# Performance work log

Hardware: AMD Instinct MI355X
Metric: run time of the kernel (lower is better)

The kernel has to match this reference:

```python
import jax, jax.numpy as jnp
import numpy as np

L, B, T, D, H = 8, 4, 1024, 1024, 16
DH = D // H
TPB, NB = 16, 64  # tokens_per_block, max_blocks; T == TPB*NB
EPS = 1e-5


def _block_causal_mask():
    idx = jnp.arange(T)
    causal = idx[:, None] >= idx[None, :]
    blk = idx // TPB
    block_diag = blk[:, None] == blk[None, :]
    return causal | block_diag  # [T, T] bool


def _ln(x, g, b):
    mu = jnp.mean(x, axis=-1, keepdims=True)
    var = jnp.mean(jnp.square(x - mu), axis=-1, keepdims=True)
    return (x - mu) * jax.lax.rsqrt(var + EPS) * g + b


def setup_inputs() -> dict:
    key = jax.random.key(0)
    ks = jax.random.split(key, 8)
    s = 0.02
    inp = {
        'sequences': jax.random.normal(ks[0], (B, T, D), jnp.float32),
        'Wq': jax.random.normal(ks[1], (L, D, D), jnp.float32) * s,
        'bq': jnp.zeros((L, D), jnp.float32),
        'Wk': jax.random.normal(ks[2], (L, D, D), jnp.float32) * s,
        'bk': jnp.zeros((L, D), jnp.float32),
        'Wv': jax.random.normal(ks[3], (L, D, D), jnp.float32) * s,
        'bv': jnp.zeros((L, D), jnp.float32),
        'Wp': jax.random.normal(ks[4], (L, D, D), jnp.float32) * s,
        'bp': jnp.zeros((L, D), jnp.float32),
        'ln1_g': jnp.ones((L, D), jnp.float32),
        'ln1_b': jnp.zeros((L, D), jnp.float32),
        'ln2_g': jnp.ones((L, D), jnp.float32),
        'ln2_b': jnp.zeros((L, D), jnp.float32),
        'W1': jax.random.normal(ks[5], (L, D, 4 * D), jnp.float32) * s,
        'b1': jnp.zeros((L, 4 * D), jnp.float32),
        'W2': jax.random.normal(ks[6], (L, 4 * D, D), jnp.float32) * s,
        'b2': jnp.zeros((L, D), jnp.float32),
        'lnf_g': jnp.ones((D,), jnp.float32),
        'lnf_b': jnp.zeros((D,), jnp.float32),
    }
    return inp


def reference(sequences, Wq, bq, Wk, bk, Wv, bv, Wp, bp,
              ln1_g, ln1_b, ln2_g, ln2_b, W1, b1, W2, b2, lnf_g, lnf_b):
    mask = _block_causal_mask()
    scale = 1.0 / np.sqrt(DH)
    x = sequences
    for i in range(L):
        h = _ln(x, ln1_g[i], ln1_b[i])
        q = (h @ Wq[i] + bq[i]).reshape(B, T, H, DH)
        k = (h @ Wk[i] + bk[i]).reshape(B, T, H, DH)
        v = (h @ Wv[i] + bv[i]).reshape(B, T, H, DH)
        att = jnp.einsum('bthd,bshd->bhts', q, k) * scale  # [B,H,T,T]
        att = jnp.where(mask, att, -jnp.inf)
        att = jax.nn.softmax(att, axis=-1)
        y = jnp.einsum('bhts,bshd->bthd', att, v).reshape(B, T, D)
        x = x + (y @ Wp[i] + bp[i])
        h2 = _ln(x, ln2_g[i], ln2_b[i])
        ff = jax.nn.gelu(h2 @ W1[i] + b1[i], approximate=False) @ W2[i] + b2[i]
        x = x + ff
    return _ln(x, lnf_g, lnf_b)
```

## Files before the change

kernel.cpp:

```cpp
#include <hip/hip_runtime.h>
#include <hip/hip_bf16.h>
#include <math.h>

#define B_ 4
#define T_ 1024
#define D_ 1024
#define H_ 16
#define DH_ 64
#define M_ 4096
#define QSTR_ 3072
#define EPS_ 1e-5f

typedef __attribute__((ext_vector_type(4))) float f32x4;
typedef __attribute__((ext_vector_type(8))) short s16x8;

#if __has_builtin(__builtin_amdgcn_exp2f)
#define EXP2F __builtin_amdgcn_exp2f
#else
#define EXP2F exp2f
#endif

__device__ __forceinline__ float gelu_f(float x) {
  return 0.5f * x * (1.0f + erff(x * 0.70710678118654752f));
}
__device__ __forceinline__ float b2f(unsigned short u) {
  union { unsigned int i; float f; } c; c.i = ((unsigned int)u) << 16; return c.f;
}
__device__ __forceinline__ unsigned short f2b(float f) {
  __hip_bfloat16 h = __float2bfloat16(f);
  return *reinterpret_cast<unsigned short*>(&h);
}
__device__ __forceinline__ void g2l16(void* l, const void* g) {
  __builtin_amdgcn_global_load_lds(
      (const __attribute__((address_space(1))) void*)g,
      (__attribute__((address_space(3))) void*)l, 16, 0, 0);
}

template<bool BF16OUT>
__global__ __launch_bounds__(256) void ln_kernel(
    const float* __restrict__ in, void* __restrict__ out,
    const float* __restrict__ g, const float* __restrict__ b) {
  const int row = blockIdx.x;
  const int tid = threadIdx.x;
  const float* rp = in + (size_t)row * D_;
  float4 v = *reinterpret_cast<const float4*>(rp + tid * 4);
  float s = v.x + v.y + v.z + v.w;
  float s2 = v.x * v.x + v.y * v.y + v.z * v.z + v.w * v.w;
#pragma unroll
  for (int off = 1; off < 64; off <<= 1) {
    s += __shfl_xor(s, off);
    s2 += __shfl_xor(s2, off);
  }
  __shared__ float red[2][4];
  const int wid = tid >> 6;
  if ((tid & 63) == 0) { red[0][wid] = s; red[1][wid] = s2; }
  __syncthreads();
  s = red[0][0] + red[0][1] + red[0][2] + red[0][3];
  s2 = red[1][0] + red[1][1] + red[1][2] + red[1][3];
  const float mu = s * (1.0f / D_);
  const float var = s2 * (1.0f / D_) - mu * mu;
  const float rs = rsqrtf(var + EPS_);
  float4 gv = *reinterpret_cast<const float4*>(g + tid * 4);
  float4 bv = *reinterpret_cast<const float4*>(b + tid * 4);
  float o0 = (v.x - mu) * rs * gv.x + bv.x;
  float o1 = (v.y - mu) * rs * gv.y + bv.y;
  float o2 = (v.z - mu) * rs * gv.z + bv.z;
  float o3 = (v.w - mu) * rs * gv.w + bv.w;
  if (BF16OUT) {
    ushort4 pk;
    pk.x = f2b(o0); pk.y = f2b(o1); pk.z = f2b(o2); pk.w = f2b(o3);
    *reinterpret_cast<ushort4*>((unsigned short*)out + (size_t)row * D_ + tid * 4) = pk;
  } else {
    *reinterpret_cast<float4*>((float*)out + (size_t)row * D_ + tid * 4) =
        make_float4(o0, o1, o2, o3);
  }
}

__global__ __launch_bounds__(256) void concat_bias(
    const float* __restrict__ bq, const float* __restrict__ bk,
    const float* __restrict__ bv, float* __restrict__ out) {
  const int i = blockIdx.x * 256 + threadIdx.x;
  const int l = i / QSTR_, c = i % QSTR_;
  const float* src = (c < 1024) ? bq : ((c < 2048) ? bk : bv);
  out[i] = src[l * 1024 + (c & 1023)];
}

__device__ __forceinline__ void transpose_tile(
    const float* __restrict__ src, int sld,
    __hip_bfloat16* __restrict__ dst, int dld, int k0, int n0) {
  __shared__ float tile[32][33];
  const int t = threadIdx.x;
  const int r = t >> 3;
  const int cq = (t & 7) * 4;
  float4 vv = *reinterpret_cast<const float4*>(src + (size_t)(k0 + r) * sld + n0 + cq);
  tile[r][cq + 0] = vv.x; tile[r][cq + 1] = vv.y;
  tile[r][cq + 2] = vv.z; tile[r][cq + 3] = vv.w;
  __syncthreads();
  ushort4 o;
  o.x = f2b(tile[cq + 0][r]); o.y = f2b(tile[cq + 1][r]);
  o.z = f2b(tile[cq + 2][r]); o.w = f2b(tile[cq + 3][r]);
  *reinterpret_cast<ushort4*>((unsigned short*)dst + (size_t)(n0 + r) * dld + k0 + cq) = o;
}

struct TrAll {
  const float *wq, *wk, *wv, *wp, *w1, *w2;
  __hip_bfloat16 *dqkv, *dp, *d1, *d2;
};

__global__ __launch_bounds__(256) void transpose_all(TrAll a) {
  const int t = blockIdx.x;
  const float* src;
  __hip_bfloat16* dst;
  int sld, dld, k0, n0;
  if (t < 4096) {
    const int m = t >> 10, tile = t & 1023;
    k0 = (tile >> 5) * 32; n0 = (tile & 31) * 32;
    src = (m == 0) ? a.wq : (m == 1) ? a.wk : (m == 2) ? a.wv : a.wp;
    sld = 1024; dld = 1024;
    dst = (m < 3) ? (a.dqkv + (size_t)m * 1024 * 1024) : a.dp;
  } else if (t < 8192) {
    const int tile = t - 4096;
    k0 = (tile & 31) * 32; n0 = (tile >> 5) * 32;
    src = a.w1; sld = 4096; dst = a.d1; dld = 1024;
  } else {
    const int tile = t - 8192;
    k0 = (tile >> 5) * 32; n0 = (tile & 31) * 32;
    src = a.w2; sld = 1024; dst = a.d2; dld = 4096;
  }
  transpose_tile(src, sld, dst, dld, k0, n0);
}

template<int MODE, int BN>
__global__ __launch_bounds__(256) void gemm_mfma(
    const __hip_bfloat16* __restrict__ A,
    const __hip_bfloat16* __restrict__ Bt,
    const float* __restrict__ bias,
    void* __restrict__ Cout, int N, int K) {
  __shared__ short As[3][128 * 32];
  __shared__ short Bs[3][BN * 32];
  int bid = blockIdx.y * gridDim.x + blockIdx.x;
  const int nwg = gridDim.x * gridDim.y;
  bid = (bid & 7) * (nwg >> 3) + (bid >> 3);
  const int gn = (bid % gridDim.x) * BN;
  const int gm = (bid / gridDim.x) * 128;

  const int tid = threadIdx.x;
  const int wid = tid >> 6, lane = tid & 63;
  constexpr int MR = (BN == 128) ? 4 : 2;
  const int wm = (BN == 128) ? (wid >> 1) : wid;
  const int wn = (BN == 128) ? (wid & 1) : 0;
  const int fr = lane & 15, kg = lane >> 4;

  const int ldr = lane >> 2;
  const int ldk = (((lane & 3) ^ ((lane >> 3) & 3)) * 8);
  const unsigned short* ap =
      (const unsigned short*)A + (size_t)(gm + wid * 32 + ldr) * K + ldk;
  const unsigned short* bp =
      (const unsigned short*)Bt +
      (size_t)(gn + ((BN == 128) ? wid * 32 : wid * 16) + ldr) * K + ldk;

  const int nkt = K >> 5;

#define STAGE_T(t, buf)                                                    \
  {                                                                        \
    const unsigned short* a_ = ap + (size_t)(t) * 32;                      \
    g2l16((char*)As[buf] + (wid * 2) * 1024, a_);                          \
    g2l16((char*)As[buf] + (wid * 2 + 1) * 1024, a_ + (size_t)16 * K);     \
    const unsigned short* b_ = bp + (size_t)(t) * 32;                      \
    if (BN == 128) {                                                       \
      g2l16((char*)Bs[buf] + (wid * 2) * 1024, b_);                        \
      g2l16((char*)Bs[buf] + (wid * 2 + 1) * 1024, b_ + (size_t)16 * K);   \
    } else {                                                               \
      g2l16((char*)Bs[buf] + wid * 1024, b_);                              \
    }                                                                      \
  }

  STAGE_T(0, 0);
  STAGE_T(1, 1);

  const int cxa = (kg ^ ((fr >> 1) & 3)) * 8;
  f32x4 acc[MR][4] = {};
  for (int t = 0; t < nkt; ++t) {
    const int buf = t % 3;
    if (t + 2 < nkt) STAGE_T(t + 2, (t + 2) % 3);
    const int rem = nkt - 1 - t;
    if (rem >= 2) {
      if (BN == 128) asm volatile("s_waitcnt vmcnt(8)" ::: "memory");
      else           asm volatile("s_waitcnt vmcnt(6)" ::: "memory");
    } else if (rem == 1) {
      if (BN == 128) asm volatile("s_waitcnt vmcnt(4)" ::: "memory");
      else           asm volatile("s_waitcnt vmcnt(3)" ::: "memory");
    } else {
      asm volatile("s_waitcnt vmcnt(0)" ::: "memory");
    }
    __builtin_amdgcn_s_barrier();
    __builtin_amdgcn_sched_barrier(0);
    s16x8 af[MR], bfr[4];
#pragma unroll
    for (int m = 0; m < MR; ++m)
      af[m] = *reinterpret_cast<const s16x8*>(
          &As[buf][(wm * (16 * MR) + m * 16 + fr) * 32 + cxa]);
#pragma unroll
    for (int n = 0; n < 4; ++n)
      bfr[n] = *reinterpret_cast<const s16x8*>(
          &Bs[buf][(wn * 64 + n * 16 + fr) * 32 + cxa]);
#pragma unroll
    for (int m = 0; m < MR; ++m)
#pragma unroll
      for (int n = 0; n < 4; ++n)
        acc[m][n] = __builtin_amdgcn_mfma_f32_16x16x32_bf16(af[m], bfr[n], acc[m][n], 0, 0, 0);
    __builtin_amdgcn_sched_barrier(0);
    __builtin_amdgcn_s_barrier();
  }
#undef STAGE_T

  const int r0 = gm + wm * (16 * MR);
  const int c0 = gn + wn * 64;
  float bb[4];
#pragma unroll
  for (int n = 0; n < 4; ++n)
    bb[n] = bias ? bias[c0 + n * 16 + fr] : 0.0f;
#pragma unroll
  for (int m = 0; m < MR; ++m) {
#pragma unroll
    for (int j = 0; j < 4; ++j) {
      const int row = r0 + m * 16 + kg * 4 + j;
#pragma unroll
      for (int n = 0; n < 4; ++n) {
        float val = acc[m][n][j] + bb[n];
        const size_t idx = (size_t)row * N + c0 + n * 16 + fr;
        if (MODE == 0) {
          ((unsigned short*)Cout)[idx] = f2b(val);
        } else if (MODE == 1) {
          float* cp = (float*)Cout + idx;
          *cp = *cp + val;
        } else {
          ((unsigned short*)Cout)[idx] = f2b(gelu_f(val));
        }
      }
    }
  }
}

__global__ __launch_bounds__(256) void attn_mfma(
    const __hip_bfloat16* __restrict__ qkv, __hip_bfloat16* __restrict__ yg) {
  const int qb = 7 - blockIdx.x;
  const int hh = blockIdx.y;
  const int bb = blockIdx.z;
  __shared__ short Qs[128 * 64];
  __shared__ short Ks[64 * 64];
  __shared__ short Vt[64 * 64];
  const int tid = threadIdx.x;
  const int wid = tid >> 6, lane = tid & 63;
  const int fr = lane & 15, kg = lane >> 4;
  const size_t qb_base = (size_t)bb * T_ * QSTR_ + (size_t)hh * DH_;
  const unsigned short* qgp = (const unsigned short*)qkv + qb_base;
  const unsigned short* kgp = qgp + 1024;
  const unsigned short* vgp = qgp + 2048;
  const float C = 0.125f * 1.4426950408889634f;

  {
    const int r8 = lane >> 3, cp = lane & 7;
#pragma unroll
    for (int u = 0; u < 4; ++u) {
      const int row = wid * 32 + u * 8 + r8;
      const int c16 = cp ^ (row & 7);
      g2l16((char*)Qs + (wid * 32 + u * 8) * 128,
            qgp + (size_t)(qb * 128 + row) * QSTR_ + c16 * 8);
    }
  }
  asm volatile("s_waitcnt vmcnt(0)" ::: "memory");
  __syncthreads();
  s16x8 qf[2][2];
#pragma unroll
  for (int rg = 0; rg < 2; ++rg) {
    const int row = wid * 32 + rg * 16 + fr;
    const char* rp = (const char*)Qs + row * 128;
    qf[rg][0] = *reinterpret_cast<const s16x8*>(rp + (((0 + kg) ^ (row & 7)) << 4));
    qf[rg][1] = *reinterpret_cast<const s16x8*>(rp + (((4 + kg) ^ (row & 7)) << 4));
  }

  f32x4 acco[2][4] = {};
  float m_run[2][4], l_run[2][4];
#pragma unroll
  for (int rg = 0; rg < 2; ++rg)
#pragma unroll
    for (int j = 0; j < 4; ++j) { m_run[rg][j] = -INFINITY; l_run[rg][j] = 0.f; }

  const int q16hi = qb * 8 + wid * 2 + 1;
  const int ntile = 2 * qb + 2;
  for (int kt = 0; kt < ntile; ++kt) {
    __syncthreads();
    {
      const int r8 = lane >> 3, cp = lane & 7;
#pragma unroll
      for (int u = 0; u < 2; ++u) {
        const int row = wid * 16 + u * 8 + r8;
        const int c16 = cp ^ (row & 7);
        g2l16((char*)Ks + (wid * 16 + u * 8) * 128,
              kgp + (size_t)(kt * 64 + row) * QSTR_ + c16 * 8);
      }
    }
    {
      const int kv0 = tid >> 3;
      const int d0 = (tid & 7) * 8;
      const int rot = tid & 7;
#pragma unroll
      for (int u = 0; u < 2; ++u) {
        const int kv = u * 32 + kv0;
        s16x8 sv = *reinterpret_cast<const s16x8*>(
            vgp + (size_t)(kt * 64 + kv) * QSTR_ + d0);
#pragma unroll
        for (int j = 0; j < 8; ++j) {
          const int jj = (j + rot) & 7;
          const int d = d0 + jj;
          *(short*)((char*)Vt + d * 128 + ((((kv >> 3) ^ jj) & 7) << 4) + (kv & 7) * 2) = sv[jj];
        }
      }
    }
    asm volatile("s_waitcnt vmcnt(0)" ::: "memory");
    __syncthreads();

    if (kt * 4 <= q16hi) {
      f32x4 accs[2][4] = {};
#pragma unroll
      for (int n = 0; n < 4; ++n) {
        const int row = n * 16 + fr;
        const char* rp = (const char*)Ks + row * 128;
        s16x8 kf0 = *reinterpret_cast<const s16x8*>(rp + (((0 + kg) ^ (row & 7)) << 4));
        s16x8 kf1 = *reinterpret_cast<const s16x8*>(rp + (((4 + kg) ^ (row & 7)) << 4));
#pragma unroll
        for (int rg = 0; rg < 2; ++rg) {
          accs[rg][n] = __builtin_amdgcn_mfma_f32_16x16x32_bf16(qf[rg][0], kf0, accs[rg][n], 0, 0, 0);
          accs[rg][n] = __builtin_amdgcn_mfma_f32_16x16x32_bf16(qf[rg][1], kf1, accs[rg][n], 0, 0, 0);
        }
      }
#pragma unroll
      for (int rg = 0; rg < 2; ++rg) {
        const int q16 = qb * 8 + wid * 2 + rg;
        float mloc[4] = {-3.0e38f, -3.0e38f, -3.0e38f, -3.0e38f};
#pragma unroll
        for (int n = 0; n < 4; ++n)
          if (kt * 4 + n <= q16)
#pragma unroll
            for (int j = 0; j < 4; ++j) mloc[j] = fmaxf(mloc[j], accs[rg][n][j]);
#pragma unroll
        for (int off = 1; off < 16; off <<= 1)
#pragma unroll
          for (int j = 0; j < 4; ++j) mloc[j] = fmaxf(mloc[j], __shfl_xor(mloc[j], off));
        float a_[4];
#pragma unroll
        for (int j = 0; j < 4; ++j) {
          const float mn = fmaxf(m_run[rg][j], mloc[j]);
          a_[j] = EXP2F((m_run[rg][j] - mn) * C);
          m_run[rg][j] = mn;
        }
        float psum[4] = {};
#pragma unroll
        for (int n = 0; n < 4; ++n) {
          const bool dead = (kt * 4 + n > q16);
          const int c16b = n * 2 + (fr >> 3);
#pragma unroll
          for (int j = 0; j < 4; ++j) {
            float p = dead ? 0.0f : EXP2F((accs[rg][n][j] - m_run[rg][j]) * C);
            psum[j] += p;
            const int row = wid * 32 + rg * 16 + kg * 4 + j;
            *(short*)((char*)Qs + row * 128 + (((c16b ^ (row & 7)) & 7) << 4) + (fr & 7) * 2) =
                (short)f2b(p);
          }
        }
#pragma unroll
        for (int j = 0; j < 4; ++j) l_run[rg][j] = l_run[rg][j] * a_[j] + psum[j];
#pragma unroll
        for (int dt = 0; dt < 4; ++dt)
#pragma unroll
          for (int j = 0; j < 4; ++j) acco[rg][dt][j] *= a_[j];
      }
#pragma unroll
      for (int rg = 0; rg < 2; ++rg) {
        const int prow = wid * 32 + rg * 16 + fr;
        const char* pp = (const char*)Qs + prow * 128;
#pragma unroll
        for (int kk = 0; kk < 2; ++kk) {
          const s16x8 pf = *reinterpret_cast<const s16x8*>(
              pp + ((((kk * 4 + kg) ^ (prow & 7)) & 7) << 4));
#pragma unroll
          for (int dt = 0; dt < 4; ++dt) {
            const int vrow = dt * 16 + fr;
            const s16x8 vf = *reinterpret_cast<const s16x8*>(
                (const char*)Vt + vrow * 128 + ((((kk * 4 + kg) ^ (vrow & 7)) & 7) << 4));
            acco[rg][dt] = __builtin_amdgcn_mfma_f32_16x16x32_bf16(pf, vf, acco[rg][dt], 0, 0, 0);
          }
        }
      }
    }
  }

#pragma unroll
  for (int off = 1; off < 16; off <<= 1)
#pragma unroll
    for (int rg = 0; rg < 2; ++rg)
#pragma unroll
      for (int j = 0; j < 4; ++j) l_run[rg][j] += __shfl_xor(l_run[rg][j], off);
  unsigned short* yp = (unsigned short*)yg + (size_t)bb * T_ * D_ + (size_t)hh * DH_;
#pragma unroll
  for (int rg = 0; rg < 2; ++rg) {
    float inv[4];
#pragma unroll
    for (int j = 0; j < 4; ++j) inv[j] = 1.0f / l_run[rg][j];
#pragma unroll
    for (int dt = 0; dt < 4; ++dt)
#pragma unroll
      for (int j = 0; j < 4; ++j) {
        const int row = qb * 128 + wid * 32 + rg * 16 + kg * 4 + j;
        yp[(size_t)row * D_ + dt * 16 + fr] = f2b(acco[rg][dt][j] * inv[j]);
      }
  }
}

extern "C" void kernel_launch(void* const* d_in, const int* in_sizes, int n_in,
                              void* d_out, int out_size, void* d_ws, size_t ws_size,
                              hipStream_t stream) {
  (void)in_sizes; (void)n_in; (void)out_size; (void)ws_size;
  const float* seq  = (const float*)d_in[0];
  const float* Wq   = (const float*)d_in[1];
  const float* bq   = (const float*)d_in[2];
  const float* Wk   = (const float*)d_in[3];
  const float* bk   = (const float*)d_in[4];
  const float* Wv   = (const float*)d_in[5];
  const float* bv   = (const float*)d_in[6];
  const float* Wp   = (const float*)d_in[7];
  const float* bp   = (const float*)d_in[8];
  const float* ln1g = (const float*)d_in[9];
  const float* ln1b = (const float*)d_in[10];
  const float* ln2g = (const float*)d_in[11];
  const float* ln2b = (const float*)d_in[12];
  const float* W1   = (const float*)d_in[13];
  const float* b1   = (const float*)d_in[14];
  const float* W2   = (const float*)d_in[15];
  const float* b2   = (const float*)d_in[16];
  const float* lnfg = (const float*)d_in[17];
  const float* lnfb = (const float*)d_in[18];

  float* x = (float*)d_out;
  char* ws = (char*)d_ws;
  const size_t MB = 1024ull * 1024ull;
  typedef __hip_bfloat16 bf16;
  bf16*  wtqkv = (bf16*)(ws + 0 * MB);
  bf16*  wtp   = (bf16*)(ws + 6 * MB);
  bf16*  wtF1  = (bf16*)(ws + 8 * MB);
  bf16*  wtF2  = (bf16*)(ws + 16 * MB);
  bf16*  hb    = (bf16*)(ws + 24 * MB);
  bf16*  qkv   = (bf16*)(ws + 32 * MB);
  bf16*  mid   = (bf16*)(ws + 56 * MB);
  float* bqkv  = (float*)(ws + 88 * MB);

  hipMemcpyAsync(x, seq, (size_t)M_ * D_ * sizeof(float), hipMemcpyDeviceToDevice, stream);

  const dim3 blk(256);
  concat_bias<<<96, blk, 0, stream>>>(bq, bk, bv, bqkv);

  for (int i = 0; i < 8; ++i) {
    const size_t wo  = (size_t)i * D_ * D_;
    const size_t vo  = (size_t)i * D_;
    const size_t w1o = (size_t)i * D_ * 4 * D_;

    ln_kernel<true><<<M_, blk, 0, stream>>>(x, hb, ln1g + vo, ln1b + vo);
    TrAll ta;
    ta.wq = Wq + wo; ta.wk = Wk + wo; ta.wv = Wv + wo; ta.wp = Wp + wo;
    ta.w1 = W1 + w1o; ta.w2 = W2 + w1o;
    ta.dqkv = wtqkv; ta.dp = wtp; ta.d1 = wtF1; ta.d2 = wtF2;
    transpose_all<<<12288, blk, 0, stream>>>(ta);
    gemm_mfma<0, 128><<<dim3(24, 32), blk, 0, stream>>>(
        hb, wtqkv, bqkv + (size_t)i * QSTR_, qkv, QSTR_, 1024);
    attn_mfma<<<dim3(8, 16, 4), blk, 0, stream>>>(qkv, hb);
    gemm_mfma<1, 64><<<dim3(16, 32), blk, 0, stream>>>(hb, wtp, bp + vo, x, 1024, 1024);
    ln_kernel<true><<<M_, blk, 0, stream>>>(x, hb, ln2g + vo, ln2b + vo);
    gemm_mfma<2, 128><<<dim3(32, 32), blk, 0, stream>>>(
        hb, wtF1, b1 + (size_t)i * 4096, mid, 4096, 1024);
    gemm_mfma<1, 64><<<dim3(16, 32), blk, 0, stream>>>(
        mid, wtF2, b2 + vo, x, 1024, 4096);
  }
  ln_kernel<false><<<M_, blk, 0, stream>>>(x, x, lnfg, lnfb);
}
```

Measured before the change: 2.292 ms.

## Split-K the FFN down-projection GEMM into two halves plus a reduction kernel

Replaces the FFN second GEMM (K=4096, 512 workgroups) with a split-K kernel that launches 1024 workgroups, each covering half of K. The first split adds its result and the bias into x, the second writes partials to a scratch buffer that reuses the qkv workspace, and a separate kernel then adds those partials into x. The aim is more parallelism and shorter per-block K loops, at the cost of an extra 16MB write, an extra read-modify-write pass over x, and one more launch per layer.

```diff
diff --git a/kernel.cpp b/kernel.cpp
--- a/kernel.cpp
+++ b/kernel.cpp
@@ -85,6 +85,15 @@
   out[i] = src[l * 1024 + (c & 1023)];
 }
 
+__global__ __launch_bounds__(256) void reduce_add(
+    float* __restrict__ x, const float* __restrict__ p) {
+  const int i = blockIdx.x * 256 + threadIdx.x;
+  float4 a = reinterpret_cast<float4*>(x)[i];
+  float4 b = reinterpret_cast<const float4*>(p)[i];
+  a.x += b.x; a.y += b.y; a.z += b.z; a.w += b.w;
+  reinterpret_cast<float4*>(x)[i] = a;
+}
+
 __device__ __forceinline__ void transpose_tile(
     const float* __restrict__ src, int sld,
     __hip_bfloat16* __restrict__ dst, int dld, int k0, int n0) {
@@ -239,6 +248,108 @@
         }
       }
     }
+  }
+}
+
+__global__ __launch_bounds__(256) void gemm_sk2(
+    const __hip_bfloat16* __restrict__ A,
+    const __hip_bfloat16* __restrict__ Bt,
+    const float* __restrict__ bias,
+    float* __restrict__ X, float* __restrict__ P,
+    int N, int K , int KS ) {
+  __shared__ short As[3][128 * 32];
+  __shared__ short Bs[3][64 * 32];
+  int bid = blockIdx.y * gridDim.x + blockIdx.x;
+  const int nwg = gridDim.x * gridDim.y;
+  bid = (bid & 7) * (nwg >> 3) + (bid >> 3);
+  const int gn = (bid % gridDim.x) * 64;
+  const int gm = (bid / gridDim.x) * 128;
+  const int koff = blockIdx.z * KS;
+
+  const int tid = threadIdx.x;
+  const int wid = tid >> 6, lane = tid & 63;
+  const int wm = wid, wn = 0;
+  const int fr = lane & 15, kg = lane >> 4;
+
+  const int ldr = lane >> 2;
+  const int ldk = (((lane & 3) ^ ((lane >> 3) & 3)) * 8);
+  const unsigned short* ap =
+      (const unsigned short*)A + (size_t)(gm + wid * 32 + ldr) * K + koff + ldk;
+  const unsigned short* bp =
+      (const unsigned short*)Bt + (size_t)(gn + wid * 16 + ldr) * K + koff + ldk;
+
+  const int nkt = KS >> 5;
+
+#define STAGE_S(t, buf)                                                    \
+  {                                                                        \
+    const unsigned short* a_ = ap + (size_t)(t) * 32;                      \
+    g2l16((char*)As[buf] + (wid * 2) * 1024, a_);                          \
+    g2l16((char*)As[buf] + (wid * 2 + 1) * 1024, a_ + (size_t)16 * K);     \
+    g2l16((char*)Bs[buf] + wid * 1024, bp + (size_t)(t) * 32);             \
+  }
+
+  STAGE_S(0, 0);
+  STAGE_S(1, 1);
+
+  const int cxa = (kg ^ ((fr >> 1) & 3)) * 8;
+  f32x4 acc[2][4] = {};
+  for (int t = 0; t < nkt; ++t) {
+    const int buf = t % 3;
+    if (t + 2 < nkt) STAGE_S(t + 2, (t + 2) % 3);
+    const int rem = nkt - 1 - t;
+    if (rem >= 2)      asm volatile("s_waitcnt vmcnt(6)" ::: "memory");
+    else if (rem == 1) asm volatile("s_waitcnt vmcnt(3)" ::: "memory");
+    else               asm volatile("s_waitcnt vmcnt(0)" ::: "memory");
+    __builtin_amdgcn_s_barrier();
+    __builtin_amdgcn_sched_barrier(0);
+    s16x8 af[2], bfr[4];
+#pragma unroll
+    for (int m = 0; m < 2; ++m)
+      af[m] = *reinterpret_cast<const s16x8*>(
+          &As[buf][(wm * 32 + m * 16 + fr) * 32 + cxa]);
+#pragma unroll
+    for (int n = 0; n < 4; ++n)
+      bfr[n] = *reinterpret_cast<const s16x8*>(
+          &Bs[buf][(wn * 64 + n * 16 + fr) * 32 + cxa]);
+#pragma unroll
+    for (int m = 0; m < 2; ++m)
+#pragma unroll
+      for (int n = 0; n < 4; ++n)
+        acc[m][n] = __builtin_amdgcn_mfma_f32_16x16x32_bf16(af[m], bfr[n], acc[m][n], 0, 0, 0);
+    __builtin_amdgcn_sched_barrier(0);
+    __builtin_amdgcn_s_barrier();
+  }
+#undef STAGE_S
+
+  const int r0 = gm + wm * 32;
+  const int c0 = gn;
+  if (blockIdx.z == 0) {
+    float bb[4];
+#pragma unroll
+    for (int n = 0; n < 4; ++n) bb[n] = bias[c0 + n * 16 + fr];
+#pragma unroll
+    for (int m = 0; m < 2; ++m)
+#pragma unroll
+      for (int j = 0; j < 4; ++j) {
+        const int row = r0 + m * 16 + kg * 4 + j;
+#pragma unroll
+        for (int n = 0; n < 4; ++n) {
+          const size_t idx = (size_t)row * N + c0 + n * 16 + fr;
+          X[idx] = X[idx] + acc[m][n][j] + bb[n];
+        }
+      }
+  } else {
+#pragma unroll
+    for (int m = 0; m < 2; ++m)
+#pragma unroll
+      for (int j = 0; j < 4; ++j) {
+        const int row = r0 + m * 16 + kg * 4 + j;
+#pragma unroll
+        for (int n = 0; n < 4; ++n) {
+          const size_t idx = (size_t)row * N + c0 + n * 16 + fr;
+          P[idx] = acc[m][n][j];
+        }
+      }
   }
 }
 
@@ -454,6 +565,7 @@
   bf16*  qkv   = (bf16*)(ws + 32 * MB);
   bf16*  mid   = (bf16*)(ws + 56 * MB);
   float* bqkv  = (float*)(ws + 88 * MB);
+  float* part  = (float*)(ws + 32 * MB);
 
   hipMemcpyAsync(x, seq, (size_t)M_ * D_ * sizeof(float), hipMemcpyDeviceToDevice, stream);
 
@@ -478,8 +590,9 @@
     ln_kernel<true><<<M_, blk, 0, stream>>>(x, hb, ln2g + vo, ln2b + vo);
     gemm_mfma<2, 128><<<dim3(32, 32), blk, 0, stream>>>(
         hb, wtF1, b1 + (size_t)i * 4096, mid, 4096, 1024);
-    gemm_mfma<1, 64><<<dim3(16, 32), blk, 0, stream>>>(
-        mid, wtF2, b2 + vo, x, 1024, 4096);
+    gemm_sk2<<<dim3(16, 32, 2), blk, 0, stream>>>(
+        mid, wtF2, b2 + vo, x, part, 1024, 4096, 2048);
+    reduce_add<<<4096, blk, 0, stream>>>(x, part);
   }
   ln_kernel<false><<<M_, blk, 0, stream>>>(x, x, lnfg, lnfb);
 }
```

Measured after the change: 2.241 ms. 2.2% less time.
